# Kernel tuning notes

Hardware: AMD Instinct MI355X
Metric: run time of the kernel (lower is better)

The kernel has to match this reference:

```python
import jax, jax.numpy as jnp
import numpy as np
import math

B, T, P, E, H = 4, 64, 256, 512, 8
D = E // H
LN_EPS = 1e-5


def setup_inputs() -> dict:
    key = jax.random.key(0)
    ks = jax.random.split(key, 6)
    s = 0.02  # weight init scale
    return {
        "x": jax.random.normal(ks[0], (B, T, P, E), jnp.float32),
        "Wq": jax.random.normal(ks[1], (E, E), jnp.float32) * s,
        "bq": jnp.zeros((E,), jnp.float32),
        "Wk": jax.random.normal(ks[2], (E, E), jnp.float32) * s,
        "bk": jnp.zeros((E,), jnp.float32),
        "Wv": jax.random.normal(ks[3], (E, E), jnp.float32) * s,
        "bv": jnp.zeros((E,), jnp.float32),
        "Wo": jax.random.normal(ks[4], (E, E), jnp.float32) * s,
        "bo": jnp.zeros((E,), jnp.float32),
        "ln_g": jnp.ones((E,), jnp.float32),
        "ln_b": jnp.zeros((E,), jnp.float32),
    }


def _proj(x, W, b):
    # torch nn.Linear: y = x @ W.T + b
    return jnp.einsum('btpe,fe->btpf', x, W) + b


def _heads(y):
    # b t p (h d) -> b p h t d
    b, t, p, e = y.shape
    return y.reshape(b, t, p, H, D).transpose(0, 2, 3, 1, 4)


def reference(x, Wq, bq, Wk, bk, Wv, bv, Wo, bo, ln_g, ln_b):
    b, t, p, e = x.shape
    q = _heads(_proj(x, Wq, bq))  # [B,P,H,T,D]
    k = _heads(_proj(x, Wk, bk))
    v = _heads(_proj(x, Wv, bv))

    scores = jnp.einsum('bphtd,bphsd->bphts', q, k) / math.sqrt(D)
    causal_mask = jnp.triu(jnp.ones((t, t), dtype=bool), k=1)  # True above diag
    scores = jnp.where(causal_mask, -jnp.inf, scores)
    attn = jax.nn.softmax(scores, axis=-1)
    o = jnp.einsum('bphts,bphsd->bphtd', attn, v)

    # b p h t d -> b t p (h d)
    o = o.transpose(0, 3, 1, 2, 4).reshape(b, t, p, e)
    attn_out = jnp.einsum('btpe,fe->btpf', o, Wo) + bo

    y = x + attn_out
    # AdaptiveNormalizer with conditioning=None -> plain LayerNorm over E
    mu = jnp.mean(y, axis=-1, keepdims=True)
    var = jnp.var(y, axis=-1, keepdims=True)
    return (y - mu) * jax.lax.rsqrt(var + LN_EPS) * ln_g + ln_b
```

## Files before the change

### kernel.cpp

```cpp
#include <hip/hip_runtime.h>
#include <stdint.h>

#define B_ 4
#define T_ 64
#define P_ 256
#define E_ 512
#define H_ 8
#define D_ 64
#define NF 1536
#define MCH 16384

typedef unsigned short u16;
typedef __attribute__((ext_vector_type(8))) __bf16 bf16x8;
typedef __attribute__((ext_vector_type(4))) float f32x4;

__device__ __forceinline__ u16 f2bf(float x) {
  union { float f; uint32_t u; } a; a.f = x;
  uint32_t u = a.u;
  uint32_t r = (u + 0x7FFFu + ((u >> 16) & 1u)) >> 16;
  return (u16)r;
}

__device__ __forceinline__ bf16x8 ld8(const u16* p) {
  union { uint4 u; bf16x8 b; } t;
  t.u = *reinterpret_cast<const uint4*>(p);
  return t.b;
}

typedef __attribute__((address_space(3))) void lds_void;
typedef __attribute__((address_space(1))) void g_void;
__device__ __forceinline__ void gl_lds16(const void* g, void* l) {
  __builtin_amdgcn_global_load_lds((g_void*)g, (lds_void*)l, 16, 0, 0);
}

__device__ __forceinline__ f32x4 mfma16(bf16x8 a, bf16x8 b, f32x4 c) {
  return __builtin_amdgcn_mfma_f32_16x16x32_bf16(a, b, c, 0, 0, 0);
}

#define SBAR() __builtin_amdgcn_s_barrier()

__global__ void cvt_bf16(const float* __restrict__ src, u16* __restrict__ dst, int n8) {
  int i = blockIdx.x * blockDim.x + threadIdx.x;
  if (i >= n8) return;
  const float4* s = reinterpret_cast<const float4*>(src) + (size_t)i * 2;
  float4 a = s[0], b = s[1];
  union { u16 u[8]; uint4 v; } t;
  t.u[0] = f2bf(a.x); t.u[1] = f2bf(a.y); t.u[2] = f2bf(a.z); t.u[3] = f2bf(a.w);
  t.u[4] = f2bf(b.x); t.u[5] = f2bf(b.y); t.u[6] = f2bf(b.z); t.u[7] = f2bf(b.w);
  reinterpret_cast<uint4*>(dst)[i] = t.v;
}

__global__ void cvt_w(const float* __restrict__ Wq, const float* __restrict__ Wk,
                      const float* __restrict__ Wv, const float* __restrict__ Wo,
                      u16* __restrict__ wqkv, u16* __restrict__ wobf) {
  int idx = blockIdx.x * blockDim.x + threadIdx.x;
  int w = idx >> 15;
  int off = idx & 32767;
  const float* s = (w == 0) ? Wq : (w == 1) ? Wk : (w == 2) ? Wv : Wo;
  const float4* sp = reinterpret_cast<const float4*>(s) + (size_t)off * 2;
  float4 a = sp[0], b = sp[1];
  union { u16 u[8]; uint4 v; } t;
  t.u[0] = f2bf(a.x); t.u[1] = f2bf(a.y); t.u[2] = f2bf(a.z); t.u[3] = f2bf(a.w);
  t.u[4] = f2bf(b.x); t.u[5] = f2bf(b.y); t.u[6] = f2bf(b.z); t.u[7] = f2bf(b.w);
  if (w < 3) reinterpret_cast<uint4*>(wqkv)[w * 32768 + off] = t.v;
  else       reinterpret_cast<uint4*>(wobf)[off] = t.v;
}

#define K1_MFMA(MB)                                                         \
  __builtin_amdgcn_s_setprio(1);                                            \
  _Pragma("unroll") for (int i = 0; i < 4; i++)                             \
  _Pragma("unroll") for (int j = 0; j < 4; j++)                             \
    acc[(MB) + i][j] = mfma16(af[i], bfv[j], acc[(MB) + i][j]);             \
  __builtin_amdgcn_s_setprio(0);

#define K1_READA(E, HH, MB)                                                 \
  _Pragma("unroll") for (int i = 0; i < 4; i++)                             \
    af[i] = ld8(ldsA + ((E) * 2 + (HH)) * 8192 +                            \
                (wr * 128 + ((MB) + i) * 16 + l15) * 32 + xr8);

#define K1_READB(E, HH)                                                     \
  _Pragma("unroll") for (int j = 0; j < 4; j++)                             \
    bfv[j] = ld8(ldsB + ((E) * 2 + (HH)) * 8192 +                           \
                 (wc * 64 + j * 16 + l15) * 32 + xr8);

__global__ __launch_bounds__(512, 2) void k1_qkv(
    const u16* __restrict__ xbf,
    const u16* __restrict__ wqkv,
    const float* __restrict__ bq, const float* __restrict__ bk, const float* __restrict__ bv,
    u16* __restrict__ qkv)
{
  __shared__ u16 lds[65536];
  u16* ldsA = lds;
  u16* ldsB = lds + 32768;

  const int tid = threadIdx.x;
  const int lane = tid & 63, wid = tid >> 6;
  const int wr = wid >> 2, wc = wid & 3;
  const int g4 = lane >> 4, l15 = lane & 15;
  const int xr8 = (g4 ^ ((l15 >> 1) & 3)) * 8;

  const int cpx = gridDim.x >> 3;
  const int logical = (blockIdx.x & 7) * cpx + (blockIdx.x >> 3);
  const int m0 = (logical / 6) * 256;
  const int n0 = (logical % 6) * 256;

  const u16* ga = xbf + (size_t)m0 * E_;
  const u16* gb = wqkv + (size_t)n0 * E_;

  const int r0 = tid >> 2;
  const int c0 = ((tid & 3) ^ ((tid >> 3) & 3)) * 8;

  auto stageA = [&](int e, int h, int kt) {
    const int kc = kt * 64 + h * 32;
    u16* base = ldsA + (e * 2 + h) * 8192;
    gl_lds16(ga + (size_t)r0 * E_ + kc + c0, base + wid * 512);
    gl_lds16(ga + (size_t)(r0 + 128) * E_ + kc + c0, base + 4096 + wid * 512);
  };
  auto stageB = [&](int e, int h, int kt) {
    const int kc = kt * 64 + h * 32;
    u16* base = ldsB + (e * 2 + h) * 8192;
    gl_lds16(gb + (size_t)r0 * E_ + kc + c0, base + wid * 512);
    gl_lds16(gb + (size_t)(r0 + 128) * E_ + kc + c0, base + 4096 + wid * 512);
  };

  f32x4 acc[8][4];
#pragma unroll
  for (int i = 0; i < 8; i++)
#pragma unroll
    for (int j = 0; j < 4; j++) { f32x4 z = {0.f, 0.f, 0.f, 0.f}; acc[i][j] = z; }

  stageA(0, 0, 0); stageB(0, 0, 0);
  stageA(0, 1, 0); stageB(0, 1, 0);
  stageA(1, 0, 1); stageB(1, 0, 1);
  asm volatile("s_waitcnt vmcnt(8)" ::: "memory");
  SBAR();

#pragma unroll 2
  for (int s = 0; s < 8; ++s) {
    const int e = s & 1;
    bf16x8 af[4], bfv[4];
    K1_READA(e, 0, 0)
    K1_READB(e, 0)
    if (s < 7) stageA(e ^ 1, 1, s + 1);
    SBAR();
    K1_MFMA(0)
    SBAR();
    K1_READA(e, 0, 4)
    if (s < 7) stageB(e ^ 1, 1, s + 1);
    if (s < 7) { asm volatile("s_waitcnt vmcnt(8)" ::: "memory"); }
    else       { asm volatile("s_waitcnt vmcnt(0)" ::: "memory"); }
    SBAR();
    K1_MFMA(4)
    SBAR();
    K1_READA(e, 1, 0)
    K1_READB(e, 1)
    if (s < 6) stageA(e, 0, s + 2);
    SBAR();
    K1_MFMA(0)
    SBAR();
    K1_READA(e, 1, 4)
    if (s < 6) stageB(e, 0, s + 2);
    if (s < 6)      { asm volatile("s_waitcnt vmcnt(8)" ::: "memory"); }
    else if (s == 6){ asm volatile("s_waitcnt vmcnt(4)" ::: "memory"); }
    SBAR();
    K1_MFMA(4)
    SBAR();
  }

  float bias4[4];
#pragma unroll
  for (int ni = 0; ni < 4; ni++) {
    const int fcol = n0 + wc * 64 + ni * 16 + l15;
    bias4[ni] = fcol < 512 ? bq[fcol] : (fcol < 1024 ? bk[fcol - 512] : bv[fcol - 1024]);
  }
  const int fbase = n0 + wc * 64 + l15;
#pragma unroll
  for (int mi = 0; mi < 8; mi++)
#pragma unroll
    for (int r = 0; r < 4; r++) {
      const size_t row = m0 + wr * 128 + mi * 16 + g4 * 4 + r;
      u16* dst = qkv + row * NF + fbase;
#pragma unroll
      for (int ni = 0; ni < 4; ni++)
        dst[ni * 16] = f2bf(acc[mi][ni][r] + bias4[ni]);
    }
}

__global__ __launch_bounds__(256) void k2_attn(
    const u16* __restrict__ qkv,
    u16* __restrict__ o)
{
  __shared__ u16 Pl[4][64 * 72];
  const int tid = threadIdx.x, lane = tid & 63, wid = tid >> 6;
  const int gw = blockIdx.x * 4 + wid;
  const int b = gw >> 11;
  const int g = gw & 2047;
  const int h = g & 7, p = g >> 3;
  const int g4 = lane >> 4;
  const size_t ts = (size_t)P_ * NF;
  const u16* qb = qkv + (size_t)b * MCH * NF + (size_t)p * NF + h * D_;
  const u16* kb = qb + 512;
  const u16* vb = qb + 1024;
  u16* ob = o + (size_t)b * MCH * E_;

  bf16x8 qf[4][2], kf[4][2];
#pragma unroll
  for (int i = 0; i < 4; i++)
#pragma unroll
    for (int ks = 0; ks < 2; ks++) {
      const int rr = i * 16 + (lane & 15);
      const int dc = ks * 32 + g4 * 8;
      qf[i][ks] = ld8(qb + (size_t)rr * ts + dc);
      kf[i][ks] = ld8(kb + (size_t)rr * ts + dc);
    }
  f32x4 S[4][4];
#pragma unroll
  for (int i = 0; i < 4; i++)
#pragma unroll
    for (int j = 0; j < 4; j++) { f32x4 z = {0.f, 0.f, 0.f, 0.f}; S[i][j] = z; }
#pragma unroll
  for (int ks = 0; ks < 2; ks++)
#pragma unroll
    for (int mi = 0; mi < 4; mi++)
#pragma unroll
      for (int ni = 0; ni < 4; ni++)
        S[mi][ni] = mfma16(qf[mi][ks], kf[ni][ks], S[mi][ni]);

  u16* pw = &Pl[wid][0];
#pragma unroll
  for (int mi = 0; mi < 4; mi++)
#pragma unroll
    for (int r = 0; r < 4; r++) {
      const int t = mi * 16 + g4 * 4 + r;
      float v[4]; float mx = -1e30f;
#pragma unroll
      for (int ni = 0; ni < 4; ni++) {
        const int s = ni * 16 + (lane & 15);
        v[ni] = (s <= t) ? S[mi][ni][r] * 0.125f : -1e30f;
        mx = fmaxf(mx, v[ni]);
      }
      mx = fmaxf(mx, __shfl_xor(mx, 1));
      mx = fmaxf(mx, __shfl_xor(mx, 2));
      mx = fmaxf(mx, __shfl_xor(mx, 4));
      mx = fmaxf(mx, __shfl_xor(mx, 8));
      float sum = 0.f; float pv[4];
#pragma unroll
      for (int ni = 0; ni < 4; ni++) {
        const int s = ni * 16 + (lane & 15);
        pv[ni] = (s <= t) ? __expf(v[ni] - mx) : 0.f;
        sum += pv[ni];
      }
      sum += __shfl_xor(sum, 1);
      sum += __shfl_xor(sum, 2);
      sum += __shfl_xor(sum, 4);
      sum += __shfl_xor(sum, 8);
      const float inv = 1.0f / sum;
#pragma unroll
      for (int ni = 0; ni < 4; ni++) {
        const int s = ni * 16 + (lane & 15);
        pw[t * 72 + s] = f2bf(pv[ni] * inv);
      }
    }
  __syncthreads();

  f32x4 O[4][4];
#pragma unroll
  for (int i = 0; i < 4; i++)
#pragma unroll
    for (int j = 0; j < 4; j++) { f32x4 z = {0.f, 0.f, 0.f, 0.f}; O[i][j] = z; }
#pragma unroll
  for (int ks = 0; ks < 2; ks++) {
    bf16x8 pa[4], vf[4];
#pragma unroll
    for (int mi = 0; mi < 4; mi++)
      pa[mi] = ld8(pw + (mi * 16 + (lane & 15)) * 72 + ks * 32 + g4 * 8);
#pragma unroll
    for (int ni = 0; ni < 4; ni++) {
      union { u16 u[8]; bf16x8 b; } tv;
#pragma unroll
      for (int j = 0; j < 8; j++) {
        const int s = ks * 32 + g4 * 8 + j;
        tv.u[j] = vb[(size_t)s * ts + ni * 16 + (lane & 15)];
      }
      vf[ni] = tv.b;
    }
#pragma unroll
    for (int mi = 0; mi < 4; mi++)
#pragma unroll
      for (int ni = 0; ni < 4; ni++)
        O[mi][ni] = mfma16(pa[mi], vf[ni], O[mi][ni]);
  }
#pragma unroll
  for (int mi = 0; mi < 4; mi++)
#pragma unroll
    for (int ni = 0; ni < 4; ni++)
#pragma unroll
      for (int r = 0; r < 4; r++) {
        const int t = mi * 16 + g4 * 4 + r;
        const int d = ni * 16 + (lane & 15);
        ob[((size_t)t * P_ + p) * E_ + h * D_ + d] = f2bf(O[mi][ni][r]);
      }
}

__global__ __launch_bounds__(512, 4) void k3_out(
    const u16* __restrict__ obf,
    const u16* __restrict__ wo,
    const float* __restrict__ bo,
    const float* __restrict__ x,
    const float* __restrict__ lng, const float* __restrict__ lnb,
    float* __restrict__ out)
{
  __shared__ u16 Bs[2][512 * 32];
  __shared__ float redS[64][8];
  __shared__ float redQ[64][8];
  const int tid = threadIdx.x, lane = tid & 63, wid = tid >> 6;
  const int g4 = lane >> 4, l15 = lane & 15;
  const int xr8 = (g4 ^ ((l15 >> 1) & 3)) * 8;
  const int m0 = blockIdx.x * 64;

  const int srow = lane >> 2;
  const int scol = ((lane & 3) ^ ((srow >> 1) & 3)) * 8;

  const u16* ga = obf + (size_t)m0 * E_;

  auto stageB = [&](int e, int kt) {
    const int k0 = kt * 32;
#pragma unroll
    for (int p = 0; p < 4; ++p) {
      const int gz = wid * 4 + p;
      gl_lds16(wo + (size_t)(gz * 16 + srow) * E_ + k0 + scol, &Bs[e][gz * 512]);
    }
  };

  f32x4 acc[4][4];
#pragma unroll
  for (int i = 0; i < 4; i++)
#pragma unroll
    for (int j = 0; j < 4; j++) { f32x4 z = {0.f, 0.f, 0.f, 0.f}; acc[i][j] = z; }

  stageB(0, 0);
  asm volatile("s_waitcnt vmcnt(0)" ::: "memory");
  SBAR();

#pragma unroll 2
  for (int kt = 0; kt < 16; ++kt) {
    const int e = kt & 1;
    bf16x8 af[4], bfv[4];
#pragma unroll
    for (int mi = 0; mi < 4; mi++)
      af[mi] = ld8(ga + (size_t)(mi * 16 + l15) * E_ + kt * 32 + g4 * 8);
    if (kt < 15) {
      stageB(e ^ 1, kt + 1);
      asm volatile("s_waitcnt vmcnt(4)" ::: "memory");
    } else {
      asm volatile("s_waitcnt vmcnt(0)" ::: "memory");
    }
    SBAR();
#pragma unroll
    for (int ni = 0; ni < 4; ni++)
      bfv[ni] = ld8(&Bs[e][(wid * 64 + ni * 16 + l15) * 32 + xr8]);
    __builtin_amdgcn_s_setprio(1);
#pragma unroll
    for (int mi = 0; mi < 4; mi++)
#pragma unroll
      for (int ni = 0; ni < 4; ni++)
        acc[mi][ni] = mfma16(af[mi], bfv[ni], acc[mi][ni]);
    __builtin_amdgcn_s_setprio(0);
    SBAR();
  }

  const int fb = wid * 64 + l15;
  float gg[4], bb[4], bof[4];
#pragma unroll
  for (int ni = 0; ni < 4; ni++) {
    const int f = fb + ni * 16;
    gg[ni] = lng[f]; bb[ni] = lnb[f]; bof[ni] = bo[f];
  }
#pragma unroll
  for (int mi = 0; mi < 4; mi++)
#pragma unroll
    for (int r = 0; r < 4; r++) {
      const int n = m0 + mi * 16 + g4 * 4 + r;
#pragma unroll
      for (int ni = 0; ni < 4; ni++)
        acc[mi][ni][r] += bof[ni] + x[(size_t)n * E_ + fb + ni * 16];
    }
#pragma unroll
  for (int mi = 0; mi < 4; mi++)
#pragma unroll
    for (int r = 0; r < 4; r++) {
      float s = 0.f, q = 0.f;
#pragma unroll
      for (int ni = 0; ni < 4; ni++) { const float y = acc[mi][ni][r]; s += y; q += y * y; }
      s += __shfl_xor(s, 1); q += __shfl_xor(q, 1);
      s += __shfl_xor(s, 2); q += __shfl_xor(q, 2);
      s += __shfl_xor(s, 4); q += __shfl_xor(q, 4);
      s += __shfl_xor(s, 8); q += __shfl_xor(q, 8);
      if (l15 == 0) {
        const int rl = mi * 16 + g4 * 4 + r;
        redS[rl][wid] = s; redQ[rl][wid] = q;
      }
    }
  __syncthreads();
#pragma unroll
  for (int mi = 0; mi < 4; mi++)
#pragma unroll
    for (int r = 0; r < 4; r++) {
      const int rl = mi * 16 + g4 * 4 + r;
      float Sx = 0.f, Qx = 0.f;
#pragma unroll
      for (int w = 0; w < 8; w++) { Sx += redS[rl][w]; Qx += redQ[rl][w]; }
      const float mean = Sx * (1.0f / 512.0f);
      const float var = Qx * (1.0f / 512.0f) - mean * mean;
      const float rs = rsqrtf(var + 1e-5f);
      const int n = m0 + rl;
#pragma unroll
      for (int ni = 0; ni < 4; ni++)
        out[(size_t)n * E_ + fb + ni * 16] = (acc[mi][ni][r] - mean) * rs * gg[ni] + bb[ni];
    }
}

extern "C" void kernel_launch(void* const* d_in, const int* in_sizes, int n_in,
                              void* d_out, int out_size, void* d_ws, size_t ws_size,
                              hipStream_t stream) {
  const float* x   = (const float*)d_in[0];
  const float* Wq  = (const float*)d_in[1];
  const float* bq  = (const float*)d_in[2];
  const float* Wk  = (const float*)d_in[3];
  const float* bk  = (const float*)d_in[4];
  const float* Wv  = (const float*)d_in[5];
  const float* bv  = (const float*)d_in[6];
  const float* Wo  = (const float*)d_in[7];
  const float* bo  = (const float*)d_in[8];
  const float* lng = (const float*)d_in[9];
  const float* lnb = (const float*)d_in[10];
  float* out = (float*)d_out;
  uint8_t* ws = (uint8_t*)d_ws;

  const size_t NEED_BIG = 270532608ULL;
  if (ws_size >= NEED_BIG) {
    u16* wqkv = (u16*)(ws);
    u16* wobf = (u16*)(ws + 1572864);
    u16* xbf  = (u16*)(ws + 2097152);
    u16* qkvc = (u16*)(ws + 69206016);
    u16* obf  = xbf;

    cvt_w<<<512, 256, 0, stream>>>(Wq, Wk, Wv, Wo, wqkv, wobf);
    cvt_bf16<<<16384, 256, 0, stream>>>(x, xbf, B_ * MCH * E_ / 8);
    k1_qkv<<<1536, 512, 0, stream>>>(xbf, wqkv, bq, bk, bv, qkvc);
    k2_attn<<<2048, 256, 0, stream>>>(qkvc, obf);
    k3_out<<<1024, 512, 0, stream>>>(obf, wobf, bo, x, lng, lnb, out);
  } else {
    u16* xbf  = (u16*)(ws);
    u16* qkvc = (u16*)(ws + 16777216);
    u16* obf  = (u16*)(ws + 67108864);
    u16* wqkv = (u16*)(ws + 83886080);
    u16* wobf = (u16*)(ws + 85458944);

    cvt_w<<<512, 256, 0, stream>>>(Wq, Wk, Wv, Wo, wqkv, wobf);
    for (int b = 0; b < B_; ++b) {
      const float* xb = x + (size_t)b * MCH * E_;
      cvt_bf16<<<4096, 256, 0, stream>>>(xb, xbf, MCH * E_ / 8);
      k1_qkv<<<384, 512, 0, stream>>>(xbf, wqkv, bq, bk, bv, qkvc);
      k2_attn<<<512, 256, 0, stream>>>(qkvc, obf);
      k3_out<<<256, 512, 0, stream>>>(obf, wobf, bo, xb, lng, lnb, out + (size_t)b * MCH * E_);
    }
  }
}
```

Baseline: 443.0 us.

## Load Wo fragments directly from global into registers, drop LDS staging

The output-projection kernel no longer stages Wo tiles through shared memory with barriers. Each wave now loads its A and B fragments straight from global memory into registers, double-buffered across K steps of 64, and interleaves those loads with the MFMAs. The launch-bounds occupancy hint drops from 4 to 2 blocks to leave room for the extra fragment registers. This removes LDS traffic and block-wide synchronisation, but each wave now fetches Wo from global or L2 separately instead of sharing one staged copy, and occupancy may fall.

```diff
diff --git a/kernel.cpp b/kernel.cpp
--- a/kernel.cpp
+++ b/kernel.cpp
@@ -302,7 +302,7 @@
       }
 }
 
-__global__ __launch_bounds__(512, 4) void k3_out(
+__global__ __launch_bounds__(512, 2) void k3_out(
     const u16* __restrict__ obf,
     const u16* __restrict__ wo,
     const float* __restrict__ bo,
@@ -310,27 +310,14 @@
     const float* __restrict__ lng, const float* __restrict__ lnb,
     float* __restrict__ out)
 {
-  __shared__ u16 Bs[2][512 * 32];
   __shared__ float redS[64][8];
   __shared__ float redQ[64][8];
   const int tid = threadIdx.x, lane = tid & 63, wid = tid >> 6;
   const int g4 = lane >> 4, l15 = lane & 15;
-  const int xr8 = (g4 ^ ((l15 >> 1) & 3)) * 8;
   const int m0 = blockIdx.x * 64;
 
-  const int srow = lane >> 2;
-  const int scol = ((lane & 3) ^ ((srow >> 1) & 3)) * 8;
-
   const u16* ga = obf + (size_t)m0 * E_;
-
-  auto stageB = [&](int e, int kt) {
-    const int k0 = kt * 32;
-#pragma unroll
-    for (int p = 0; p < 4; ++p) {
-      const int gz = wid * 4 + p;
-      gl_lds16(wo + (size_t)(gz * 16 + srow) * E_ + k0 + scol, &Bs[e][gz * 512]);
-    }
-  };
+  const u16* gb = wo + (size_t)(wid * 64) * E_;
 
   f32x4 acc[4][4];
 #pragma unroll
@@ -338,35 +325,30 @@
 #pragma unroll
     for (int j = 0; j < 4; j++) { f32x4 z = {0.f, 0.f, 0.f, 0.f}; acc[i][j] = z; }
 
-  stageB(0, 0);
-  asm volatile("s_waitcnt vmcnt(0)" ::: "memory");
-  SBAR();
-
-#pragma unroll 2
-  for (int kt = 0; kt < 16; ++kt) {
-    const int e = kt & 1;
-    bf16x8 af[4], bfv[4];
-#pragma unroll
-    for (int mi = 0; mi < 4; mi++)
-      af[mi] = ld8(ga + (size_t)(mi * 16 + l15) * E_ + kt * 32 + g4 * 8);
-    if (kt < 15) {
-      stageB(e ^ 1, kt + 1);
-      asm volatile("s_waitcnt vmcnt(4)" ::: "memory");
-    } else {
-      asm volatile("s_waitcnt vmcnt(0)" ::: "memory");
-    }
-    SBAR();
-#pragma unroll
-    for (int ni = 0; ni < 4; ni++)
-      bfv[ni] = ld8(&Bs[e][(wid * 64 + ni * 16 + l15) * 32 + xr8]);
-    __builtin_amdgcn_s_setprio(1);
-#pragma unroll
-    for (int mi = 0; mi < 4; mi++)
-#pragma unroll
-      for (int ni = 0; ni < 4; ni++)
-        acc[mi][ni] = mfma16(af[mi], bfv[ni], acc[mi][ni]);
-    __builtin_amdgcn_s_setprio(0);
-    SBAR();
+  bf16x8 afA[4][2], afB[4][2], bfA[4][2], bfB[4][2];
+
+#define K3_LOADA(AF, T)                                                     \
+  _Pragma("unroll") for (int mi = 0; mi < 4; mi++)                          \
+  _Pragma("unroll") for (int ks = 0; ks < 2; ks++)                          \
+    AF[mi][ks] = ld8(ga + (size_t)(mi * 16 + l15) * E_ + (T) * 64 + ks * 32 + g4 * 8);
+#define K3_LOADB(BF, T)                                                     \
+  _Pragma("unroll") for (int ni = 0; ni < 4; ni++)                          \
+  _Pragma("unroll") for (int ks = 0; ks < 2; ks++)                          \
+    BF[ni][ks] = ld8(gb + (size_t)(ni * 16 + l15) * E_ + (T) * 64 + ks * 32 + g4 * 8);
+#define K3_COMP(AF, BF)                                                     \
+  _Pragma("unroll") for (int ks = 0; ks < 2; ks++)                          \
+  _Pragma("unroll") for (int mi = 0; mi < 4; mi++)                          \
+  _Pragma("unroll") for (int ni = 0; ni < 4; ni++)                          \
+    acc[mi][ni] = mfma16(AF[mi][ks], BF[ni][ks], acc[mi][ni]);
+
+  K3_LOADA(afA, 0)
+  K3_LOADB(bfA, 0)
+#pragma unroll
+  for (int t = 0; t < 8; t += 2) {
+    if (t + 1 < 8) { K3_LOADA(afB, t + 1) K3_LOADB(bfB, t + 1) }
+    K3_COMP(afA, bfA)
+    if (t + 2 < 8) { K3_LOADA(afA, t + 2) K3_LOADB(bfA, t + 2) }
+    if (t + 1 < 8) { K3_COMP(afB, bfB) }
   }
 
   const int fb = wid * 64 + l15;
```

Result: faster. 398.3 us (-10.1%).
